# Performance work log

Hardware: AMD Instinct MI355X
Metric: run time of the kernel (lower is better)

Reference implementation:

```python
import jax, jax.numpy as jnp
import numpy as np

B, LQ, LK = 4, 2048, 2048
DQ, DK, DO = 1024, 1024, 1024


def setup_inputs() -> dict:
    key = jax.random.key(0)
    ks = jax.random.split(key, 9)
    s = 0.02
    return {
        "query_input": jax.random.normal(ks[0], (B, LQ, DQ), jnp.float32),
        "key_input": jax.random.normal(ks[1], (B, LK, DK), jnp.float32),
        "value_input": jax.random.normal(ks[2], (B, LK, DK), jnp.float32),
        "Wq": jax.random.normal(ks[3], (DQ, DO), jnp.float32) * s,
        "bq": jax.random.normal(ks[4], (DO,), jnp.float32) * s,
        "Wk": jax.random.normal(ks[5], (DK, DO), jnp.float32) * s,
        "bk": jax.random.normal(ks[6], (DO,), jnp.float32) * s,
        "Wv": jax.random.normal(ks[7], (DK, DO), jnp.float32) * s,
        "bv": jax.random.normal(ks[8], (DO,), jnp.float32) * s,
    }


def reference(query_input, key_input, value_input, Wq, bq, Wk, bk, Wv, bv):
    scale = jnp.asarray(DO, query_input.dtype) ** 0.5
    q = query_input @ Wq + bq              # [B, Lq, D]
    k = key_input @ Wk + bk                # [B, Lk, D]
    v = value_input @ Wv + bv              # [B, Lk, D]
    attn = jnp.einsum("bqd,bkd->bqk", q, k) / scale
    attn = jax.nn.softmax(attn, axis=-1)
    return jnp.einsum("bqk,bkd->bqd", attn, v)
```

## Files before the change

### kernel.cpp

```cpp
#include <hip/hip_runtime.h>

typedef _Float16 f16x8 __attribute__((ext_vector_type(8)));
typedef _Float16 f16x4 __attribute__((ext_vector_type(4)));
typedef float f32x4 __attribute__((ext_vector_type(4)));

__device__ __forceinline__ void lds_load16(const _Float16* g, _Float16* l) {
    __builtin_amdgcn_global_load_lds(
        (const __attribute__((address_space(1))) void*)g,
        (__attribute__((address_space(3))) void*)l,
        16, 0, 0);
}

template <int MODE>
__global__ __launch_bounds__(512, 2)
void gemm_core(const _Float16* A0, const _Float16* B0, void* C0, const float* b0,
               const _Float16* A1, const _Float16* B1, void* C1, const float* b1,
               const _Float16* A2, const _Float16* B2, void* C2, const float* b2,
               float* rowsum)
{
    constexpr int K   = (MODE == 5) ? 2048 : 1024;
    constexpr int LDA = (MODE == 5) ? 2048 : 1024;
    constexpr int LDB = (MODE == 5) ? 8192 : 1024;
    constexpr int NT  = K / 64;

    __shared__ __align__(16) _Float16 As[2][256 * 64];
    __shared__ __align__(16) _Float16 Bs[2][256 * 64];

    const int z = blockIdx.z;
    const int bx = blockIdx.x, by = blockIdx.y;
    const int t    = threadIdx.x;
    const int w    = t >> 6;
    const int lane = t & 63;
    const int ln   = lane & 15;
    const int kq   = lane >> 4;
    const int wm   = (w >> 2) * 128;
    const int wn   = (w & 3) * 64;

    const _Float16* A;
    const _Float16* B;
    size_t cbase = 0;
    int m0, n0;

    if (MODE == 0) {
        A = z == 0 ? A0 : z == 1 ? A1 : A2;
        B = z == 0 ? B0 : z == 1 ? B1 : B2;
        if (z == 2) { m0 = (by & 3) * 256;             n0 = (bx * 4 + (by >> 2)) * 256; }
        else        { m0 = (bx * 4 + (by >> 2)) * 256; n0 = (by & 3) * 256; }
    } else if (MODE == 3) {
        A = A0 + (size_t)z * 2048 * 1024;
        B = B0 + (size_t)z * 2048 * 1024;
        cbase = (size_t)z * 2048 * 2048;
        rowsum += z * 2048;
        m0 = ((bx & 3) * 2 + (by >> 2)) * 256;
        n0 = ((bx >> 2) * 4 + (by & 3)) * 256;
    } else {
        A = A0 + (size_t)z * 2048 * 2048;
        B = B0 + (size_t)z * 2048;
        cbase = (size_t)z * 2048 * 1024;
        rowsum += z * 2048;
        m0 = bx * 256;
        n0 = by * 256;
    }

    const int l3 = lane >> 3;
    const int lc = ((lane & 7) ^ l3) * 8;
    const _Float16* gA = A + (size_t)(m0 + w * 16 + l3) * LDA + lc;
    const _Float16* gB = B + (size_t)(n0 + w * 16 + l3) * LDB + lc;

    auto stA = [&](int b, int kt, int h) {
        const _Float16* g = gA + (size_t)(h * 128) * LDA + kt * 64;
        _Float16* l = As[b] + h * 8192 + w * 1024;
        lds_load16(g, l);
        lds_load16(g + (size_t)8 * LDA, l + 512);
    };
    auto stB = [&](int b, int kt, int h) {
        const _Float16* g = gB + (size_t)(h * 128) * LDB + kt * 64;
        _Float16* l = Bs[b] + h * 8192 + w * 1024;
        lds_load16(g, l);
        lds_load16(g + (size_t)8 * LDB, l + 512);
    };

    const int xr  = ln & 7;
    const int sk0 = ((0 + kq) ^ xr) * 8;
    const int sk1 = ((4 + kq) ^ xr) * 8;
    const int ra  = (wm + ln) * 64;
    const int rb  = (wn + ln) * 64;

    f16x8 af[4][2], bf[4][2];
    f32x4 acc[8][4] = {};

    stA(0, 0, 0); stA(0, 0, 1); stB(0, 0, 0); stB(0, 0, 1);

    for (int kt = 0; kt < NT; kt += 2) {
#pragma unroll
        for (int hlf = 0; hlf < 2; ++hlf) {
            const int  b  = hlf;
            const int  kc = kt + hlf;
            const bool pf = (kc + 1 < NT);
            const _Float16* Ab = As[b];
            const _Float16* Bb = Bs[b];

            if (pf) {
                stA(b ^ 1, kc + 1, 0); stA(b ^ 1, kc + 1, 1);
                asm volatile("s_waitcnt vmcnt(4)" ::: "memory");
            } else {
                asm volatile("s_waitcnt vmcnt(0)" ::: "memory");
            }
            __builtin_amdgcn_s_barrier();
            __builtin_amdgcn_sched_barrier(0);
#pragma unroll
            for (int i = 0; i < 4; ++i) {
                af[i][0] = *(const f16x8*)(Ab + ra + i * 1024 + sk0);
                af[i][1] = *(const f16x8*)(Ab + ra + i * 1024 + sk1);
            }
#pragma unroll
            for (int j = 0; j < 2; ++j) {
                bf[j][0] = *(const f16x8*)(Bb + rb + j * 1024 + sk0);
                bf[j][1] = *(const f16x8*)(Bb + rb + j * 1024 + sk1);
            }
            asm volatile("s_waitcnt lgkmcnt(0)" ::: "memory");
            __builtin_amdgcn_sched_barrier(0);
            __builtin_amdgcn_s_setprio(1);
#pragma unroll
            for (int i = 0; i < 4; ++i)
#pragma unroll
                for (int j = 0; j < 2; ++j) {
                    acc[i][j] = __builtin_amdgcn_mfma_f32_16x16x32_f16(af[i][0], bf[j][0], acc[i][j], 0, 0, 0);
                    acc[i][j] = __builtin_amdgcn_mfma_f32_16x16x32_f16(af[i][1], bf[j][1], acc[i][j], 0, 0, 0);
                }
            __builtin_amdgcn_s_setprio(0);
            __builtin_amdgcn_s_barrier();
            __builtin_amdgcn_sched_barrier(0);

#pragma unroll
            for (int j = 2; j < 4; ++j) {
                bf[j][0] = *(const f16x8*)(Bb + rb + j * 1024 + sk0);
                bf[j][1] = *(const f16x8*)(Bb + rb + j * 1024 + sk1);
            }
            if (pf) { stB(b ^ 1, kc + 1, 0); stB(b ^ 1, kc + 1, 1); }
            __builtin_amdgcn_s_barrier();
            asm volatile("s_waitcnt lgkmcnt(0)" ::: "memory");
            __builtin_amdgcn_sched_barrier(0);
            __builtin_amdgcn_s_setprio(1);
#pragma unroll
            for (int i = 0; i < 4; ++i)
#pragma unroll
                for (int j = 2; j < 4; ++j) {
                    acc[i][j] = __builtin_amdgcn_mfma_f32_16x16x32_f16(af[i][0], bf[j][0], acc[i][j], 0, 0, 0);
                    acc[i][j] = __builtin_amdgcn_mfma_f32_16x16x32_f16(af[i][1], bf[j][1], acc[i][j], 0, 0, 0);
                }
            __builtin_amdgcn_s_setprio(0);
            __builtin_amdgcn_s_barrier();
            __builtin_amdgcn_sched_barrier(0);

#pragma unroll
            for (int i = 0; i < 4; ++i) {
                af[i][0] = *(const f16x8*)(Ab + ra + (i + 4) * 1024 + sk0);
                af[i][1] = *(const f16x8*)(Ab + ra + (i + 4) * 1024 + sk1);
            }
            __builtin_amdgcn_s_barrier();
            asm volatile("s_waitcnt lgkmcnt(0)" ::: "memory");
            __builtin_amdgcn_sched_barrier(0);
            __builtin_amdgcn_s_setprio(1);
#pragma unroll
            for (int i = 0; i < 4; ++i)
#pragma unroll
                for (int j = 0; j < 2; ++j) {
                    acc[i + 4][j] = __builtin_amdgcn_mfma_f32_16x16x32_f16(af[i][0], bf[j][0], acc[i + 4][j], 0, 0, 0);
                    acc[i + 4][j] = __builtin_amdgcn_mfma_f32_16x16x32_f16(af[i][1], bf[j][1], acc[i + 4][j], 0, 0, 0);
                }
            __builtin_amdgcn_s_setprio(0);
            __builtin_amdgcn_s_barrier();
            __builtin_amdgcn_sched_barrier(0);

            __builtin_amdgcn_s_setprio(1);
#pragma unroll
            for (int i = 0; i < 4; ++i)
#pragma unroll
                for (int j = 2; j < 4; ++j) {
                    acc[i + 4][j] = __builtin_amdgcn_mfma_f32_16x16x32_f16(af[i][0], bf[j][0], acc[i + 4][j], 0, 0, 0);
                    acc[i + 4][j] = __builtin_amdgcn_mfma_f32_16x16x32_f16(af[i][1], bf[j][1], acc[i + 4][j], 0, 0, 0);
                }
            __builtin_amdgcn_s_setprio(0);
            __builtin_amdgcn_s_barrier();
            __builtin_amdgcn_sched_barrier(0);
        }
    }

    if (MODE == 0) {
        _Float16* Cp = (_Float16*)(z == 0 ? C0 : z == 1 ? C1 : C2);
        const float* bp = z == 0 ? b0 : z == 1 ? b1 : b2;
        const int ldc = (z == 2) ? 8192 : 1024;
#pragma unroll
        for (int i = 0; i < 8; ++i) {
            const int rbase = m0 + wm + i * 16 + kq * 4;
#pragma unroll
            for (int j = 0; j < 4; ++j) {
                const int gcol = n0 + wn + j * 16 + ln;
#pragma unroll
                for (int r = 0; r < 4; ++r) {
                    float vv = acc[i][j][r] + (z == 2 ? bp[rbase + r] : bp[gcol]);
                    Cp[(size_t)(rbase + r) * ldc + gcol] = (_Float16)vv;
                }
            }
        }
    } else if (MODE == 3) {
        _Float16* Ch = (_Float16*)C0;
#pragma unroll
        for (int i = 0; i < 8; ++i) {
            const int rbase = m0 + wm + i * 16 + kq * 4;
            float rs[4] = {0.f, 0.f, 0.f, 0.f};
#pragma unroll
            for (int j = 0; j < 4; ++j) {
                const int gcol = n0 + wn + j * 16 + ln;
#pragma unroll
                for (int r = 0; r < 4; ++r) {
                    float e = __expf(acc[i][j][r] * 0.03125f);
                    Ch[cbase + (size_t)(rbase + r) * 2048 + gcol] = (_Float16)e;
                    rs[r] += e;
                }
            }
#pragma unroll
            for (int r = 0; r < 4; ++r) {
                float s = rs[r];
                s += __shfl_xor(s, 1);
                s += __shfl_xor(s, 2);
                s += __shfl_xor(s, 4);
                s += __shfl_xor(s, 8);
                if (ln == 0) atomicAdd(&rowsum[rbase + r], s);
            }
        }
    } else {
        float* Cf = (float*)C0;
#pragma unroll
        for (int i = 0; i < 8; ++i) {
            const int rbase = m0 + wm + i * 16 + kq * 4;
            float inv[4];
#pragma unroll
            for (int r = 0; r < 4; ++r) inv[r] = 1.f / rowsum[rbase + r];
#pragma unroll
            for (int j = 0; j < 4; ++j) {
                const int gcol = n0 + wn + j * 16 + ln;
#pragma unroll
                for (int r = 0; r < 4; ++r)
                    Cf[cbase + (size_t)(rbase + r) * 1024 + gcol] = acc[i][j][r] * inv[r];
            }
        }
    }
}

__global__ __launch_bounds__(256)
void prep(const float4* __restrict__ x0, _Float16* __restrict__ y0,
          const float4* __restrict__ x1, _Float16* __restrict__ y1,
          const float4* __restrict__ x2, _Float16* __restrict__ y2,
          const float* __restrict__ W0, _Float16* __restrict__ T0,
          const float* __restrict__ W1, _Float16* __restrict__ T1,
          const float* __restrict__ W2, _Float16* __restrict__ T2,
          float* __restrict__ rowsum)
{
    if (blockIdx.y < 3) {
        const size_t i = (size_t)blockIdx.x * 256 + threadIdx.x;
        const float4* x = blockIdx.y == 0 ? x0 : blockIdx.y == 1 ? x1 : x2;
        _Float16*    yy = blockIdx.y == 0 ? y0 : blockIdx.y == 1 ? y1 : y2;
        float4 f = x[i];
        f16x4 o = { (_Float16)f.x, (_Float16)f.y, (_Float16)f.z, (_Float16)f.w };
        *(f16x4*)(yy + i * 4) = o;
        if (blockIdx.y == 0 && blockIdx.x < 32)
            rowsum[blockIdx.x * 256 + threadIdx.x] = 0.f;
        return;
    }
    if (blockIdx.x >= 3072) return;
    const int zz = blockIdx.x >> 10;
    const int tb = blockIdx.x & 1023;
    const float* W = zz == 0 ? W0 : zz == 1 ? W1 : W2;
    _Float16*   WT = zz == 0 ? T0 : zz == 1 ? T1 : T2;
    __shared__ float tile[32][33];
    const int bxs = (tb & 31) * 32;
    const int bys = (tb >> 5) * 32;
    const int tx = threadIdx.x & 31;
    const int ty = threadIdx.x >> 5;
#pragma unroll
    for (int i = ty; i < 32; i += 8)
        tile[i][tx] = W[(size_t)(bys + i) * 1024 + bxs + tx];
    __syncthreads();
#pragma unroll
    for (int i = ty; i < 32; i += 8)
        WT[(size_t)(bxs + i) * 1024 + bys + tx] = (_Float16)tile[tx][i];
}

extern "C" void kernel_launch(void* const* d_in, const int* in_sizes, int n_in,
                              void* d_out, int out_size, void* d_ws, size_t ws_size,
                              hipStream_t stream)
{
    const float* Xq = (const float*)d_in[0];
    const float* Xk = (const float*)d_in[1];
    const float* Xv = (const float*)d_in[2];
    const float* Wq = (const float*)d_in[3];
    const float* bq = (const float*)d_in[4];
    const float* Wk = (const float*)d_in[5];
    const float* bk = (const float*)d_in[6];
    const float* Wv = (const float*)d_in[7];
    const float* bv = (const float*)d_in[8];
    float* out = (float*)d_out;

    const size_t XN = (size_t)8192 * 1024;
    const size_t WN = (size_t)1024 * 1024;

    _Float16* ws  = (_Float16*)d_ws;
    _Float16* Xqh = ws;
    _Float16* Xkh = Xqh + XN;
    _Float16* Xvh = Xkh + XN;
    _Float16* WqT = Xvh + XN;
    _Float16* WkT = WqT + WN;
    _Float16* WvT = WkT + WN;
    _Float16* qh  = WvT + WN;
    _Float16* kh  = qh + XN;
    _Float16* vT  = kh + XN;
    _Float16* S   = vT + XN;
    float* rowsum = (float*)(S + (size_t)4 * 2048 * 2048);

    {
        dim3 g(8192, 4);
        prep<<<g, 256, 0, stream>>>((const float4*)Xq, Xqh,
                                    (const float4*)Xk, Xkh,
                                    (const float4*)Xv, Xvh,
                                    Wq, WqT, Wk, WkT, Wv, WvT, rowsum);
    }

    {
        dim3 g(8, 16, 3);
        gemm_core<0><<<g, 512, 0, stream>>>(
            Xqh, WqT, qh, bq,
            Xkh, WkT, kh, bk,
            WvT, Xvh, vT, bv,
            nullptr);
    }

    {
        dim3 g(8, 8, 4);
        gemm_core<3><<<g, 512, 0, stream>>>(
            qh, kh, S, nullptr,
            nullptr, nullptr, nullptr, nullptr,
            nullptr, nullptr, nullptr, nullptr,
            rowsum);
    }

    {
        dim3 g(8, 4, 4);
        gemm_core<5><<<g, 512, 0, stream>>>(
            S, vT, out, nullptr,
            nullptr, nullptr, nullptr, nullptr,
            nullptr, nullptr, nullptr, nullptr,
            rowsum);
    }
}
```

Before: 341.5 us.

## Use 128-row tiles for PV GEMM and restructure loads into a two-stage prefetch pipeline

The final S·V GEMM now uses 128x256 tiles with a regrid, giving 256 blocks instead of 128 for better CU occupancy. The K-loop is restructured so each stage loads its full A and B tiles together, issued two iterations ahead with a single staging lambda and vmcnt waits. This replaces the split A/B prefetch that ran one step ahead. It is meant to hide global load latency better and fill the machine in the last GEMM, at the cost of lower per-block reuse for MODE 5.

```diff
diff --git a/kernel.cpp b/kernel.cpp
--- a/kernel.cpp
+++ b/kernel.cpp
@@ -18,28 +18,34 @@
                const _Float16* A2, const _Float16* B2, void* C2, const float* b2,
                float* rowsum)
 {
+    constexpr int BM  = (MODE == 5) ? 128 : 256;
+    constexpr int BN  = 256;
     constexpr int K   = (MODE == 5) ? 2048 : 1024;
     constexpr int LDA = (MODE == 5) ? 2048 : 1024;
     constexpr int LDB = (MODE == 5) ? 8192 : 1024;
     constexpr int NT  = K / 64;
-
-    __shared__ __align__(16) _Float16 As[2][256 * 64];
-    __shared__ __align__(16) _Float16 Bs[2][256 * 64];
-
-    const int z = blockIdx.z;
+    constexpr int MI  = BM / 32;
+    constexpr int MH  = MI / 2;
+    constexpr int LA  = BM / 64;
+    constexpr int LT  = LA + 4;
+
+    __shared__ __align__(16) _Float16 As[2][BM * 64];
+    __shared__ __align__(16) _Float16 Bs[2][BN * 64];
+
+    const int z_ = blockIdx.z;
     const int bx = blockIdx.x, by = blockIdx.y;
     const int t    = threadIdx.x;
     const int w    = t >> 6;
     const int lane = t & 63;
     const int ln   = lane & 15;
     const int kq   = lane >> 4;
-    const int wm   = (w >> 2) * 128;
+    const int wm   = (w >> 2) * (BM / 2);
     const int wn   = (w & 3) * 64;
 
     const _Float16* A;
     const _Float16* B;
     size_t cbase = 0;
-    int m0, n0;
+    int m0, n0, z = z_;
 
     if (MODE == 0) {
         A = z == 0 ? A0 : z == 1 ? A1 : A2;
@@ -54,30 +60,27 @@
         m0 = ((bx & 3) * 2 + (by >> 2)) * 256;
         n0 = ((bx >> 2) * 4 + (by & 3)) * 256;
     } else {
+        z = (blockIdx.z << 1) | (bx >> 2);
         A = A0 + (size_t)z * 2048 * 2048;
         B = B0 + (size_t)z * 2048;
         cbase = (size_t)z * 2048 * 1024;
         rowsum += z * 2048;
-        m0 = bx * 256;
-        n0 = by * 256;
-    }
-
-    const int l3 = lane >> 3;
-    const int lc = ((lane & 7) ^ l3) * 8;
-    const _Float16* gA = A + (size_t)(m0 + w * 16 + l3) * LDA + lc;
-    const _Float16* gB = B + (size_t)(n0 + w * 16 + l3) * LDB + lc;
-
-    auto stA = [&](int b, int kt, int h) {
-        const _Float16* g = gA + (size_t)(h * 128) * LDA + kt * 64;
-        _Float16* l = As[b] + h * 8192 + w * 1024;
-        lds_load16(g, l);
-        lds_load16(g + (size_t)8 * LDA, l + 512);
-    };
-    auto stB = [&](int b, int kt, int h) {
-        const _Float16* g = gB + (size_t)(h * 128) * LDB + kt * 64;
-        _Float16* l = Bs[b] + h * 8192 + w * 1024;
-        lds_load16(g, l);
-        lds_load16(g + (size_t)8 * LDB, l + 512);
+        m0 = by * 128;
+        n0 = (bx & 3) * 256;
+    }
+
+    const int r6 = t >> 3;
+    const int cw = ((t & 7) ^ (r6 & 7)) * 8;
+    const _Float16* gA = A + (size_t)(m0 + r6) * LDA + cw;
+    const _Float16* gB = B + (size_t)(n0 + r6) * LDB + cw;
+
+    auto stage = [&](int b, int kt) {
+#pragma unroll
+        for (int s = 0; s < LA; ++s)
+            lds_load16(gA + (size_t)(s * 64) * LDA + kt * 64, As[b] + s * 4096 + w * 512);
+#pragma unroll
+        for (int s = 0; s < 4; ++s)
+            lds_load16(gB + (size_t)(s * 64) * LDB + kt * 64, Bs[b] + s * 4096 + w * 512);
     };
 
     const int xr  = ln & 7;
@@ -86,105 +89,107 @@
     const int ra  = (wm + ln) * 64;
     const int rb  = (wn + ln) * 64;
 
-    f16x8 af[4][2], bf[4][2];
-    f32x4 acc[8][4] = {};
-
-    stA(0, 0, 0); stA(0, 0, 1); stB(0, 0, 0); stB(0, 0, 1);
-
-    for (int kt = 0; kt < NT; kt += 2) {
-#pragma unroll
-        for (int hlf = 0; hlf < 2; ++hlf) {
-            const int  b  = hlf;
-            const int  kc = kt + hlf;
-            const bool pf = (kc + 1 < NT);
-            const _Float16* Ab = As[b];
-            const _Float16* Bb = Bs[b];
-
-            if (pf) {
-                stA(b ^ 1, kc + 1, 0); stA(b ^ 1, kc + 1, 1);
-                asm volatile("s_waitcnt vmcnt(4)" ::: "memory");
-            } else {
-                asm volatile("s_waitcnt vmcnt(0)" ::: "memory");
-            }
-            __builtin_amdgcn_s_barrier();
-            __builtin_amdgcn_sched_barrier(0);
-#pragma unroll
-            for (int i = 0; i < 4; ++i) {
-                af[i][0] = *(const f16x8*)(Ab + ra + i * 1024 + sk0);
-                af[i][1] = *(const f16x8*)(Ab + ra + i * 1024 + sk1);
-            }
+    f16x8 af[MH][2], bf[4][2];
+    f32x4 acc[MI][4] = {};
+
+    stage(0, 0);
+    stage(1, 1);
+    if constexpr (MODE == 5) asm volatile("s_waitcnt vmcnt(6)" ::: "memory");
+    else                     asm volatile("s_waitcnt vmcnt(8)" ::: "memory");
+    __builtin_amdgcn_s_barrier();
+    __builtin_amdgcn_sched_barrier(0);
+
+#pragma unroll 2
+    for (int kc = 0; kc < NT; ++kc) {
+        const int b = kc & 1;
+        const _Float16* Ab = As[b];
+        const _Float16* Bb = Bs[b];
+
+#pragma unroll
+        for (int i = 0; i < MH; ++i) {
+            af[i][0] = *(const f16x8*)(Ab + ra + i * 1024 + sk0);
+            af[i][1] = *(const f16x8*)(Ab + ra + i * 1024 + sk1);
+        }
+#pragma unroll
+        for (int j = 0; j < 2; ++j) {
+            bf[j][0] = *(const f16x8*)(Bb + rb + j * 1024 + sk0);
+            bf[j][1] = *(const f16x8*)(Bb + rb + j * 1024 + sk1);
+        }
+        __builtin_amdgcn_s_barrier();
+        asm volatile("s_waitcnt lgkmcnt(0)" ::: "memory");
+        __builtin_amdgcn_sched_barrier(0);
+        __builtin_amdgcn_s_setprio(1);
+#pragma unroll
+        for (int i = 0; i < MH; ++i)
 #pragma unroll
             for (int j = 0; j < 2; ++j) {
-                bf[j][0] = *(const f16x8*)(Bb + rb + j * 1024 + sk0);
-                bf[j][1] = *(const f16x8*)(Bb + rb + j * 1024 + sk1);
-            }
-            asm volatile("s_waitcnt lgkmcnt(0)" ::: "memory");
-            __builtin_amdgcn_sched_barrier(0);
-            __builtin_amdgcn_s_setprio(1);
-#pragma unroll
-            for (int i = 0; i < 4; ++i)
-#pragma unroll
-                for (int j = 0; j < 2; ++j) {
-                    acc[i][j] = __builtin_amdgcn_mfma_f32_16x16x32_f16(af[i][0], bf[j][0], acc[i][j], 0, 0, 0);
-                    acc[i][j] = __builtin_amdgcn_mfma_f32_16x16x32_f16(af[i][1], bf[j][1], acc[i][j], 0, 0, 0);
-                }
-            __builtin_amdgcn_s_setprio(0);
-            __builtin_amdgcn_s_barrier();
-            __builtin_amdgcn_sched_barrier(0);
-
+                acc[i][j] = __builtin_amdgcn_mfma_f32_16x16x32_f16(af[i][0], bf[j][0], acc[i][j], 0, 0, 0);
+                acc[i][j] = __builtin_amdgcn_mfma_f32_16x16x32_f16(af[i][1], bf[j][1], acc[i][j], 0, 0, 0);
+            }
+        __builtin_amdgcn_s_setprio(0);
+        __builtin_amdgcn_s_barrier();
+        __builtin_amdgcn_sched_barrier(0);
+
+#pragma unroll
+        for (int j = 2; j < 4; ++j) {
+            bf[j][0] = *(const f16x8*)(Bb + rb + j * 1024 + sk0);
+            bf[j][1] = *(const f16x8*)(Bb + rb + j * 1024 + sk1);
+        }
+        __builtin_amdgcn_s_barrier();
+        asm volatile("s_waitcnt lgkmcnt(0)" ::: "memory");
+        __builtin_amdgcn_sched_barrier(0);
+        __builtin_amdgcn_s_setprio(1);
+#pragma unroll
+        for (int i = 0; i < MH; ++i)
 #pragma unroll
             for (int j = 2; j < 4; ++j) {
-                bf[j][0] = *(const f16x8*)(Bb + rb + j * 1024 + sk0);
-                bf[j][1] = *(const f16x8*)(Bb + rb + j * 1024 + sk1);
-            }
-            if (pf) { stB(b ^ 1, kc + 1, 0); stB(b ^ 1, kc + 1, 1); }
-            __builtin_amdgcn_s_barrier();
-            asm volatile("s_waitcnt lgkmcnt(0)" ::: "memory");
-            __builtin_amdgcn_sched_barrier(0);
-            __builtin_amdgcn_s_setprio(1);
-#pragma unroll
-            for (int i = 0; i < 4; ++i)
-#pragma unroll
-                for (int j = 2; j < 4; ++j) {
-                    acc[i][j] = __builtin_amdgcn_mfma_f32_16x16x32_f16(af[i][0], bf[j][0], acc[i][j], 0, 0, 0);
-                    acc[i][j] = __builtin_amdgcn_mfma_f32_16x16x32_f16(af[i][1], bf[j][1], acc[i][j], 0, 0, 0);
-                }
-            __builtin_amdgcn_s_setprio(0);
-            __builtin_amdgcn_s_barrier();
-            __builtin_amdgcn_sched_barrier(0);
-
-#pragma unroll
-            for (int i = 0; i < 4; ++i) {
-                af[i][0] = *(const f16x8*)(Ab + ra + (i + 4) * 1024 + sk0);
-                af[i][1] = *(const f16x8*)(Ab + ra + (i + 4) * 1024 + sk1);
-            }
-            __builtin_amdgcn_s_barrier();
-            asm volatile("s_waitcnt lgkmcnt(0)" ::: "memory");
-            __builtin_amdgcn_sched_barrier(0);
-            __builtin_amdgcn_s_setprio(1);
-#pragma unroll
-            for (int i = 0; i < 4; ++i)
-#pragma unroll
-                for (int j = 0; j < 2; ++j) {
-                    acc[i + 4][j] = __builtin_amdgcn_mfma_f32_16x16x32_f16(af[i][0], bf[j][0], acc[i + 4][j], 0, 0, 0);
-                    acc[i + 4][j] = __builtin_amdgcn_mfma_f32_16x16x32_f16(af[i][1], bf[j][1], acc[i + 4][j], 0, 0, 0);
-                }
-            __builtin_amdgcn_s_setprio(0);
-            __builtin_amdgcn_s_barrier();
-            __builtin_amdgcn_sched_barrier(0);
-
-            __builtin_amdgcn_s_setprio(1);
-#pragma unroll
-            for (int i = 0; i < 4; ++i)
-#pragma unroll
-                for (int j = 2; j < 4; ++j) {
-                    acc[i + 4][j] = __builtin_amdgcn_mfma_f32_16x16x32_f16(af[i][0], bf[j][0], acc[i + 4][j], 0, 0, 0);
-                    acc[i + 4][j] = __builtin_amdgcn_mfma_f32_16x16x32_f16(af[i][1], bf[j][1], acc[i + 4][j], 0, 0, 0);
-                }
-            __builtin_amdgcn_s_setprio(0);
-            __builtin_amdgcn_s_barrier();
-            __builtin_amdgcn_sched_barrier(0);
-        }
+                acc[i][j] = __builtin_amdgcn_mfma_f32_16x16x32_f16(af[i][0], bf[j][0], acc[i][j], 0, 0, 0);
+                acc[i][j] = __builtin_amdgcn_mfma_f32_16x16x32_f16(af[i][1], bf[j][1], acc[i][j], 0, 0, 0);
+            }
+        __builtin_amdgcn_s_setprio(0);
+        __builtin_amdgcn_s_barrier();
+        __builtin_amdgcn_sched_barrier(0);
+
+#pragma unroll
+        for (int i = 0; i < MH; ++i) {
+            af[i][0] = *(const f16x8*)(Ab + ra + (i + MH) * 1024 + sk0);
+            af[i][1] = *(const f16x8*)(Ab + ra + (i + MH) * 1024 + sk1);
+        }
+        __builtin_amdgcn_s_barrier();
+        asm volatile("s_waitcnt lgkmcnt(0)" ::: "memory");
+        __builtin_amdgcn_sched_barrier(0);
+        __builtin_amdgcn_s_setprio(1);
+#pragma unroll
+        for (int i = 0; i < MH; ++i)
+#pragma unroll
+            for (int j = 0; j < 2; ++j) {
+                acc[i + MH][j] = __builtin_amdgcn_mfma_f32_16x16x32_f16(af[i][0], bf[j][0], acc[i + MH][j], 0, 0, 0);
+                acc[i + MH][j] = __builtin_amdgcn_mfma_f32_16x16x32_f16(af[i][1], bf[j][1], acc[i + MH][j], 0, 0, 0);
+            }
+        __builtin_amdgcn_s_setprio(0);
+        __builtin_amdgcn_s_barrier();
+        __builtin_amdgcn_sched_barrier(0);
+
+        if (kc + 2 < NT) {
+            stage(b, kc + 2);
+            if constexpr (MODE == 5) asm volatile("s_waitcnt vmcnt(6)" ::: "memory");
+            else                     asm volatile("s_waitcnt vmcnt(8)" ::: "memory");
+        } else if (kc + 1 < NT) {
+            asm volatile("s_waitcnt vmcnt(0)" ::: "memory");
+        }
+        __builtin_amdgcn_s_barrier();
+        __builtin_amdgcn_sched_barrier(0);
+        __builtin_amdgcn_s_setprio(1);
+#pragma unroll
+        for (int i = 0; i < MH; ++i)
+#pragma unroll
+            for (int j = 2; j < 4; ++j) {
+                acc[i + MH][j] = __builtin_amdgcn_mfma_f32_16x16x32_f16(af[i][0], bf[j][0], acc[i + MH][j], 0, 0, 0);
+                acc[i + MH][j] = __builtin_amdgcn_mfma_f32_16x16x32_f16(af[i][1], bf[j][1], acc[i + MH][j], 0, 0, 0);
+            }
+        __builtin_amdgcn_s_setprio(0);
+        __builtin_amdgcn_s_barrier();
+        __builtin_amdgcn_sched_barrier(0);
     }
 
     if (MODE == 0) {
@@ -192,7 +197,7 @@
         const float* bp = z == 0 ? b0 : z == 1 ? b1 : b2;
         const int ldc = (z == 2) ? 8192 : 1024;
 #pragma unroll
-        for (int i = 0; i < 8; ++i) {
+        for (int i = 0; i < MI; ++i) {
             const int rbase = m0 + wm + i * 16 + kq * 4;
 #pragma unroll
             for (int j = 0; j < 4; ++j) {
@@ -207,7 +212,7 @@
     } else if (MODE == 3) {
         _Float16* Ch = (_Float16*)C0;
 #pragma unroll
-        for (int i = 0; i < 8; ++i) {
+        for (int i = 0; i < MI; ++i) {
             const int rbase = m0 + wm + i * 16 + kq * 4;
             float rs[4] = {0.f, 0.f, 0.f, 0.f};
 #pragma unroll
@@ -233,7 +238,7 @@
     } else {
         float* Cf = (float*)C0;
 #pragma unroll
-        for (int i = 0; i < 8; ++i) {
+        for (int i = 0; i < MI; ++i) {
             const int rbase = m0 + wm + i * 16 + kq * 4;
             float inv[4];
 #pragma unroll
@@ -346,7 +351,7 @@
     }
 
     {
-        dim3 g(8, 4, 4);
+        dim3 g(8, 16, 2);
         gemm_core<5><<<g, 512, 0, stream>>>(
             S, vT, out, nullptr,
             nullptr, nullptr, nullptr, nullptr,
```

Result: faster. 319.7 us (-6.4%).
